# Optimization experiments

Measured on AMD Instinct MI355X. Metric: run time of the kernel, lower is better.

## Reference

```python
import jax, jax.numpy as jnp
import numpy as np

B, N, D = 2, 2048, 1024
H = 16
HD = D // H  # 64
N_CTX = 256


def setup_inputs() -> dict:
    key = jax.random.key(0)
    ks = jax.random.split(key, 10)
    x = jax.random.normal(ks[0], (B, N, D), dtype=jnp.float32)
    ctx_ppr = jax.random.uniform(ks[1], (N_CTX,), dtype=jnp.float32, minval=1e-4, maxval=1.0)
    ctx_trust = jax.random.uniform(ks[2], (N_CTX,), dtype=jnp.float32)
    attn_mask = jax.random.randint(ks[3], (N, N), 0, 2).astype(jnp.bool_)
    # parameters (nn.Linear convention: y = x @ W.T + b)
    s_in = 1.0 / np.sqrt(D)
    W_in = jax.random.uniform(ks[4], (3 * D, D), dtype=jnp.float32, minval=-s_in, maxval=s_in)
    b_in = jax.random.uniform(ks[5], (3 * D,), dtype=jnp.float32, minval=-s_in, maxval=s_in)
    W_out = jax.random.uniform(ks[6], (D, D), dtype=jnp.float32, minval=-s_in, maxval=s_in)
    b_out = jax.random.uniform(ks[7], (D,), dtype=jnp.float32, minval=-s_in, maxval=s_in)
    log_ppr_alpha = jnp.ones((1,), jnp.float32) * 0.1
    trust_scale = jnp.ones((1,), jnp.float32) * 0.1
    return {"x": x, "ctx_ppr": ctx_ppr, "ctx_trust": ctx_trust, "n_ctx": N_CTX,
            "attn_mask": attn_mask, "W_in": W_in, "b_in": b_in,
            "W_out": W_out, "b_out": b_out,
            "log_ppr_alpha": log_ppr_alpha, "trust_scale": trust_scale}


def reference(x, ctx_ppr, ctx_trust, n_ctx, attn_mask, W_in, b_in, W_out, b_out,
              log_ppr_alpha, trust_scale):
    Bx, Nx, Dx = x.shape
    scale = HD ** -0.5
    qkv = x @ W_in.T + b_in  # [B,N,3D]
    q, k, v = jnp.split(qkv, 3, axis=-1)
    q = q.reshape(Bx, Nx, H, HD).transpose(0, 2, 1, 3)  # [B,H,N,d]
    k = k.reshape(Bx, Nx, H, HD).transpose(0, 2, 1, 3)
    v = v.reshape(Bx, Nx, H, HD).transpose(0, 2, 1, 3)
    if n_ctx > 0:
        gate = jax.nn.sigmoid(trust_scale[0] * ctx_trust)  # [n_ctx]
        gate_full = jnp.concatenate([gate, jnp.ones(Nx - n_ctx, x.dtype)])
        v = v * gate_full[None, None, :, None]
    logits = jnp.einsum('bhqd,bhkd->bhqk', q, k) * scale
    if n_ctx > 0:
        bias = log_ppr_alpha[0] * jnp.log(jnp.clip(ctx_ppr, 1e-8, None))
        col_bias = jnp.concatenate([bias, jnp.zeros(Nx - n_ctx, x.dtype)])
        logits = logits + col_bias[None, None, None, :]
    logits = jnp.where(attn_mask[None, None, :, :], -jnp.inf, logits)
    weights = jax.nn.softmax(logits, axis=-1)
    out = jnp.einsum('bhqk,bhkd->bhqd', weights, v)
    out = out.transpose(0, 2, 1, 3).reshape(Bx, Nx, Dx)
    return out @ W_out.T + b_out
```

## Files before the change

### kernel.cpp

```cpp
#include <hip/hip_runtime.h>
#include <hip/hip_bf16.h>
#include <math.h>

#define B_   2
#define N_   2048
#define D_   1024
#define H_   16
#define TD_  3072
#define LOG2E 1.44269504088896340736f
#define SCALE_Q (0.125f * LOG2E)

typedef short  bf16x8 __attribute__((ext_vector_type(8)));
typedef _Float16 f16x8 __attribute__((ext_vector_type(8)));
typedef float  f32x4  __attribute__((ext_vector_type(4)));
typedef float  f32x16 __attribute__((ext_vector_type(16)));

#define MFMA16(a, b, c)   __builtin_amdgcn_mfma_f32_16x16x32_bf16(a, b, c, 0, 0, 0)
#define MFMA32B(a, b, c)  __builtin_amdgcn_mfma_f32_32x32x16_bf16(a, b, c, 0, 0, 0)
#define MFMA32H(a, b, c)  __builtin_amdgcn_mfma_f32_32x32x16_f16(a, b, c, 0, 0, 0)

__device__ __forceinline__ ushort f2bf(float f) {
    union { float f; unsigned u; } v; v.f = f;
    unsigned r = (v.u + 0x7fffu + ((v.u >> 16) & 1u)) >> 16;
    return (ushort)r;
}
__device__ __forceinline__ unsigned pkrtz(float a, float b) {
    typedef __fp16 h2 __attribute__((ext_vector_type(2)));
    union { h2 h; unsigned u; } c;
    c.h = __builtin_amdgcn_cvt_pkrtz(a, b);
    return c.u;
}
__device__ __forceinline__ void async16(const void* g, void* l) {
    __builtin_amdgcn_global_load_lds(
        (const __attribute__((address_space(1))) unsigned*)g,
        (__attribute__((address_space(3))) unsigned*)l, 16, 0, 0);
}

__global__ __launch_bounds__(256) void preprocess(
    const float* __restrict__ x, const float* __restrict__ W_in,
    const float* __restrict__ W_out, const float* __restrict__ ctx_ppr,
    const float* __restrict__ log_alpha, const int* __restrict__ n_ctx_p,
    const int* __restrict__ mask,
    ushort* __restrict__ xb, ushort* __restrict__ wib, ushort* __restrict__ wob,
    float* __restrict__ biasrow, unsigned* __restrict__ maskbits)
{
    const int J0 = 1048576, J1 = 786432, J2 = 262144, JM = 131072, JB = 2048;
    int t = blockIdx.x * 256 + threadIdx.x;
    if (t < J0 + J1 + J2) {
        const float* src; ushort* dst; int i = t;
        if (i < J0)           { src = x;      dst = xb;  }
        else if (i < J0 + J1) { i -= J0;      src = W_in;  dst = wib; }
        else                  { i -= J0 + J1; src = W_out; dst = wob; }
        float4 v = ((const float4*)src)[i];
        ushort4 o;
        o.x = f2bf(v.x); o.y = f2bf(v.y); o.z = f2bf(v.z); o.w = f2bf(v.w);
        ((ushort4*)dst)[i] = o;
    } else if (t < J0 + J1 + J2 + JM) {
        int i = t - (J0 + J1 + J2);
        const int4* m = (const int4*)(mask + (size_t)i * 32);
        unsigned bits = 0u;
        #pragma unroll
        for (int j = 0; j < 8; ++j) {
            int4 w = m[j];
            bits |= (w.x != 0 ? 1u : 0u) << (j * 4 + 0);
            bits |= (w.y != 0 ? 1u : 0u) << (j * 4 + 1);
            bits |= (w.z != 0 ? 1u : 0u) << (j * 4 + 2);
            bits |= (w.w != 0 ? 1u : 0u) << (j * 4 + 3);
        }
        maskbits[i] = bits;
    } else if (t < J0 + J1 + J2 + JM + JB) {
        int k = t - (J0 + J1 + J2 + JM);
        int nc = n_ctx_p[0];
        float bv = 0.f;
        if (k < nc) bv = log_alpha[0] * __log2f(fmaxf(ctx_ppr[k], 1e-8f));
        biasrow[k] = bv;
    }
}

template<int BCOL, int MODE>
__global__ __launch_bounds__(256) void gemm_bt(
    const ushort* __restrict__ A, const ushort* __restrict__ Bw,
    const float* __restrict__ bias, float* __restrict__ Cout,
    ushort* __restrict__ qkout, _Float16* __restrict__ vTout,
    int Ncol, int K,
    const float* __restrict__ ctx_trust, const float* __restrict__ trust_scale,
    const int* __restrict__ n_ctx_p)
{
    constexpr int NT = BCOL / 32;
    __shared__ ushort tA[128 * 32];
    __shared__ ushort tB[BCOL * 32];
    const int tid = threadIdx.x;
    const int lane = tid & 63, wv = tid >> 6;
    const int ln = lane & 15, kg = lane >> 4;
    const int rh = wv >> 1, ch = wv & 1;
    const int row0 = blockIdx.y * 128, col0 = blockIdx.x * BCOL;

    int offA[4], offB[NT];
    #pragma unroll
    for (int i = 0; i < 4; ++i) {
        int ra = rh * 64 + i * 16 + ln;
        offA[i] = ra * 32 + ((kg ^ ((ra >> 1) & 3)) << 3);
    }
    #pragma unroll
    for (int i = 0; i < NT; ++i) {
        int rb = ch * (BCOL / 2) + i * 16 + ln;
        offB[i] = rb * 32 + ((kg ^ ((rb >> 1) & 3)) << 3);
    }
    f32x4 acc[4][NT];
    #pragma unroll
    for (int i = 0; i < 4; ++i)
        #pragma unroll
        for (int j = 0; j < NT; ++j) acc[i][j] = (f32x4){0.f, 0.f, 0.f, 0.f};

    for (int kt = 0; kt < K; kt += 32) {
        __syncthreads();
        #pragma unroll
        for (int r2 = 0; r2 < 2; ++r2) {
            int g = r2 * 256 + tid;
            int row = g >> 2;
            int srck = ((g & 3) ^ ((row >> 1) & 3)) << 3;
            async16(A + (size_t)(row0 + row) * K + kt + srck, &tA[g * 8]);
        }
        #pragma unroll
        for (int r2 = 0; r2 < BCOL / 64; ++r2) {
            int g = r2 * 256 + tid;
            int row = g >> 2;
            int srck = ((g & 3) ^ ((row >> 1) & 3)) << 3;
            async16(Bw + (size_t)(col0 + row) * K + kt + srck, &tB[g * 8]);
        }
        __syncthreads();
        bf16x8 af[4], bfr[NT];
        #pragma unroll
        for (int i = 0; i < 4; ++i)  af[i]  = *(const bf16x8*)&tA[offA[i]];
        #pragma unroll
        for (int i = 0; i < NT; ++i) bfr[i] = *(const bf16x8*)&tB[offB[i]];
        #pragma unroll
        for (int mt = 0; mt < 4; ++mt)
            #pragma unroll
            for (int nt = 0; nt < NT; ++nt)
                acc[mt][nt] = MFMA16(af[mt], bfr[nt], acc[mt][nt]);
    }

    const int nctx = n_ctx_p ? n_ctx_p[0] : 0;
    const float ts = trust_scale ? trust_scale[0] : 0.f;
    #pragma unroll
    for (int nt = 0; nt < NT; ++nt) {
        int col = col0 + ch * (BCOL / 2) + nt * 16 + ln;
        float bv = bias[col];
        #pragma unroll
        for (int mt = 0; mt < 4; ++mt) {
            int rbase = row0 + rh * 64 + mt * 16 + kg * 4;
            f32x4 a = acc[mt][nt];
            if (MODE == 0) {
                #pragma unroll
                for (int reg = 0; reg < 4; ++reg)
                    Cout[(size_t)(rbase + reg) * Ncol + col] = a[reg] + bv;
            } else {
                if (col < D_) {
                    #pragma unroll
                    for (int reg = 0; reg < 4; ++reg)
                        qkout[(size_t)(rbase + reg) * 2048 + col] =
                            f2bf((a[reg] + bv) * SCALE_Q);
                } else if (col < 2 * D_) {
                    #pragma unroll
                    for (int reg = 0; reg < 4; ++reg)
                        qkout[(size_t)(rbase + reg) * 2048 + col] = f2bf(a[reg] + bv);
                } else {
                    int vc = col - 2 * D_;
                    int hh = vc >> 6, dim = vc & 63;
                    int bb = rbase >> 11, nbase = rbase & (N_ - 1);
                    ushort4 o;
                    #pragma unroll
                    for (int reg = 0; reg < 4; ++reg) {
                        float v = a[reg] + bv;
                        int n = nbase + reg;
                        if (n < nctx) {
                            float g = 1.f / (1.f + __expf(-ts * ctx_trust[n]));
                            v *= g;
                        }
                        _Float16 hv = (_Float16)v;
                        ((ushort*)&o)[reg] = *(ushort*)&hv;
                    }
                    *(ushort4*)&vTout[((size_t)(bb * 16 + hh) * 64 + dim) * 2048 + nbase] = o;
                }
            }
        }
    }
}

__global__ __launch_bounds__(256) void attn(
    const ushort* __restrict__ qkb,
    const _Float16* __restrict__ vT,
    const unsigned* __restrict__ maskbits,
    const float* __restrict__ biasrow,
    const int* __restrict__ n_ctx_p,
    ushort* __restrict__ attb)
{
    __shared__ ushort   Kt[2][64 * 64];
    __shared__ _Float16 Vt[2][64 * 64];
    const int tid = threadIdx.x;
    const int lane = tid & 63, wv = tid >> 6;
    const int q31 = lane & 31, hi = lane >> 5;
    const int b = blockIdx.y >> 4, h = blockIdx.y & 15;
    const int q0w = blockIdx.x * 128 + wv * 32;
    const int nctx = n_ctx_p[0];

    bf16x8 qf[4];
    {
        const ushort* qrow = qkb + (size_t)(b * N_ + q0w + q31) * 2048 + h * 64;
        #pragma unroll
        for (int ks = 0; ks < 4; ++ks)
            qf[ks] = *(const bf16x8*)(qrow + ks * 16 + hi * 8);
    }
    const size_t kgbase = (size_t)(b * N_) * 2048 + 1024 + h * 64;
    const _Float16* vbase = vT + (size_t)((b * 16 + h) * 64) * 2048;

    f32x16 O[2];
    O[0] = (f32x16)(0.f); O[1] = (f32x16)(0.f);
    float lrun = 0.f;

    {
        #pragma unroll
        for (int r2 = 0; r2 < 2; ++r2) {
            int g = r2 * 256 + tid; int row = g >> 3; int sg = (g & 7) ^ (row & 7);
            async16(qkb + kgbase + (size_t)row * 2048 + sg * 8, &Kt[0][g * 8]);
        }
        #pragma unroll
        for (int r2 = 0; r2 < 2; ++r2) {
            int g = r2 * 256 + tid; int row = g >> 3; int sg = (g & 7) ^ (row & 7);
            async16(vbase + (size_t)row * 2048 + sg * 8, &Vt[0][g * 8]);
        }
    }

    const int swz = q31 & 7;
    for (int ci = 0; ci < 32; ++ci) {
        const int c0 = ci * 64;
        __syncthreads();
        if (ci < 31) {
            const int c1 = c0 + 64, nb = (ci + 1) & 1;
            #pragma unroll
            for (int r2 = 0; r2 < 2; ++r2) {
                int g = r2 * 256 + tid; int row = g >> 3; int sg = (g & 7) ^ (row & 7);
                async16(qkb + kgbase + (size_t)(c1 + row) * 2048 + sg * 8, &Kt[nb][g * 8]);
            }
            #pragma unroll
            for (int r2 = 0; r2 < 2; ++r2) {
                int g = r2 * 256 + tid; int row = g >> 3; int sg = (g & 7) ^ (row & 7);
                async16(vbase + (size_t)row * 2048 + c1 + sg * 8, &Vt[nb][g * 8]);
            }
        }
        const ushort*   KT = Kt[ci & 1];
        const _Float16* VT = Vt[ci & 1];

        f32x16 S[2];
        S[0] = (f32x16)(0.f); S[1] = (f32x16)(0.f);
        #pragma unroll
        for (int t = 0; t < 2; ++t) {
            const int rbase = (t * 32 + q31) * 64;
            #pragma unroll
            for (int ks = 0; ks < 4; ++ks) {
                bf16x8 kf = *(const bf16x8*)&KT[rbase + (((ks * 2 + hi) ^ swz) << 3)];
                S[t] = MFMA32B(kf, qf[ks], S[t]);
            }
        }

        uint2 mw = *(const uint2*)&maskbits[(size_t)(q0w + q31) * 64 + ci * 2];
        unsigned msh[2] = { mw.x >> (hi * 4), mw.y >> (hi * 4) };
        unsigned pk[2][8];
        float lsum = 0.f;
        const bool has_bias = (c0 < nctx);
        #pragma unroll
        for (int t = 0; t < 2; ++t) {
            float p[16];
            #pragma unroll
            for (int g = 0; g < 4; ++g) {
                f32x4 bb = (f32x4){0.f, 0.f, 0.f, 0.f};
                if (has_bias)
                    bb = *(const f32x4*)&biasrow[c0 + t * 32 + g * 8 + hi * 4];
                #pragma unroll
                for (int r = 0; r < 4; ++r) {
                    const int reg = g * 4 + r;
                    const int br = r + 8 * g;
                    float s = S[t][reg] + bb[r] - 4.f;
                    s = ((msh[t] >> br) & 1u) ? -1e30f : s;
                    p[reg] = __builtin_exp2f(s);
                }
            }
            float l0 = (p[0] + p[1]) + (p[2] + p[3]);
            float l1 = (p[4] + p[5]) + (p[6] + p[7]);
            float l2 = (p[8] + p[9]) + (p[10] + p[11]);
            float l3 = (p[12] + p[13]) + (p[14] + p[15]);
            lsum += (l0 + l1) + (l2 + l3);
            #pragma unroll
            for (int i = 0; i < 8; ++i)
                pk[t][i] = pkrtz(p[2 * i], p[2 * i + 1]);
        }
        lrun += lsum;

        #pragma unroll
        for (int ks = 0; ks < 4; ++ks) {
            const int t = ks >> 1, lo4 = (ks & 1) * 4;
            unsigned u0 = pk[t][lo4 + 0], u1 = pk[t][lo4 + 1];
            unsigned u2 = pk[t][lo4 + 2], u3 = pk[t][lo4 + 3];
            unsigned own0 = hi ? u2 : u0, own1 = hi ? u3 : u1;
            unsigned snd0 = hi ? u0 : u2, snd1 = hi ? u1 : u3;
            unsigned rv0 = (unsigned)__shfl_xor((int)snd0, 32);
            unsigned rv1 = (unsigned)__shfl_xor((int)snd1, 32);
            union { f16x8 v; unsigned u[4]; } frag;
            frag.u[0] = hi ? rv0 : own0;
            frag.u[1] = hi ? rv1 : own1;
            frag.u[2] = hi ? own0 : rv0;
            frag.u[3] = hi ? own1 : rv1;
            #pragma unroll
            for (int t2 = 0; t2 < 2; ++t2) {
                const int vb = (t2 * 32 + q31) * 64;
                union { f16x8 v; int4 i; } vf;
                vf.i = *(const int4*)&VT[vb + (((ks * 2 + hi) ^ swz) << 3)];
                O[t2] = MFMA32H(vf.v, frag.v, O[t2]);
            }
        }
    }

    float l = lrun + __shfl_xor(lrun, 32);
    float inv = 1.f / l;
    ushort* orow = attb + (size_t)(b * N_ + q0w + q31) * 1024 + h * 64;
    #pragma unroll
    for (int t = 0; t < 2; ++t)
        #pragma unroll
        for (int g = 0; g < 4; ++g) {
            ushort4 o;
            #pragma unroll
            for (int r = 0; r < 4; ++r)
                ((ushort*)&o)[r] = f2bf(O[t][g * 4 + r] * inv);
            *(ushort4*)&orow[t * 32 + g * 8 + hi * 4] = o;
        }
}

extern "C" void kernel_launch(void* const* d_in, const int* in_sizes, int n_in,
                              void* d_out, int out_size, void* d_ws, size_t ws_size,
                              hipStream_t stream)
{
    const float* x         = (const float*)d_in[0];
    const float* ctx_ppr   = (const float*)d_in[1];
    const float* ctx_trust = (const float*)d_in[2];
    const int*   n_ctx_p   = (const int*)d_in[3];
    const int*   attn_mask = (const int*)d_in[4];
    const float* W_in      = (const float*)d_in[5];
    const float* b_in      = (const float*)d_in[6];
    const float* W_out     = (const float*)d_in[7];
    const float* b_out     = (const float*)d_in[8];
    const float* log_alpha = (const float*)d_in[9];
    const float* trust_sc  = (const float*)d_in[10];
    float* out = (float*)d_out;

    char* ws = (char*)d_ws;
    ushort*    xb       = (ushort*)ws;    ws += (size_t)4096 * 1024 * 2;
    ushort*    wib      = (ushort*)ws;    ws += (size_t)3072 * 1024 * 2;
    ushort*    wob      = (ushort*)ws;    ws += (size_t)1024 * 1024 * 2;
    ushort*    qkb      = (ushort*)ws;    ws += (size_t)4096 * 2048 * 2;
    _Float16*  vT       = (_Float16*)ws;  ws += (size_t)2048 * 2048 * 2;
    ushort*    attbuf   = (ushort*)ws;    ws += (size_t)4096 * 1024 * 2;
    float*     biasrow  = (float*)ws;     ws += 2048 * 4;
    unsigned*  maskbits = (unsigned*)ws;  ws += (size_t)2048 * 64 * 4;

    hipLaunchKernelGGL(preprocess, dim3(8712), dim3(256), 0, stream,
                       x, W_in, W_out, ctx_ppr, log_alpha, n_ctx_p, attn_mask,
                       xb, wib, wob, biasrow, maskbits);

    hipLaunchKernelGGL((gemm_bt<128, 1>), dim3(24, 32), dim3(256), 0, stream,
                       xb, wib, b_in, (float*)nullptr, qkb, vT, TD_, 1024,
                       ctx_trust, trust_sc, n_ctx_p);

    hipLaunchKernelGGL(attn, dim3(16, 32), dim3(256), 0, stream,
                       qkb, vT, maskbits, biasrow, n_ctx_p, attbuf);

    hipLaunchKernelGGL((gemm_bt<64, 0>), dim3(16, 32), dim3(256), 0, stream,
                       attbuf, wob, b_out, out, (ushort*)nullptr, (_Float16*)nullptr,
                       1024, 1024, ctx_trust, trust_sc, n_ctx_p);
}
```

Measured before the change: 268.7 us.

## Split attention over two key halves and merge partials in a combine kernel

```diff
diff --git a/kernel.cpp b/kernel.cpp
--- a/kernel.cpp
+++ b/kernel.cpp
@@ -12,6 +12,7 @@
 
 typedef short  bf16x8 __attribute__((ext_vector_type(8)));
 typedef _Float16 f16x8 __attribute__((ext_vector_type(8)));
+typedef _Float16 f16x4 __attribute__((ext_vector_type(4)));
 typedef float  f32x4  __attribute__((ext_vector_type(4)));
 typedef float  f32x16 __attribute__((ext_vector_type(16)));
 
@@ -34,6 +35,10 @@
     __builtin_amdgcn_global_load_lds(
         (const __attribute__((address_space(1))) unsigned*)g,
         (__attribute__((address_space(3))) unsigned*)l, 16, 0, 0);
+}
+__device__ __forceinline__ void plswap(unsigned &a, unsigned &b) {
+    auto r = __builtin_amdgcn_permlane32_swap((int)a, (int)b, false, false);
+    a = (unsigned)r[0]; b = (unsigned)r[1];
 }
 
 __global__ __launch_bounds__(256) void preprocess(
@@ -194,7 +199,9 @@
     const unsigned* __restrict__ maskbits,
     const float* __restrict__ biasrow,
     const int* __restrict__ n_ctx_p,
-    ushort* __restrict__ attb)
+    _Float16* __restrict__ op0,
+    _Float16* __restrict__ op1,
+    float* __restrict__ lpart)
 {
     __shared__ ushort   Kt[2][64 * 64];
     __shared__ _Float16 Vt[2][64 * 64];
@@ -203,6 +210,8 @@
     const int q31 = lane & 31, hi = lane >> 5;
     const int b = blockIdx.y >> 4, h = blockIdx.y & 15;
     const int q0w = blockIdx.x * 128 + wv * 32;
+    const int kh = blockIdx.z;
+    const int kbase = kh << 10;
     const int nctx = n_ctx_p[0];
 
     bf16x8 qf[4];
@@ -212,8 +221,8 @@
         for (int ks = 0; ks < 4; ++ks)
             qf[ks] = *(const bf16x8*)(qrow + ks * 16 + hi * 8);
     }
-    const size_t kgbase = (size_t)(b * N_) * 2048 + 1024 + h * 64;
-    const _Float16* vbase = vT + (size_t)((b * 16 + h) * 64) * 2048;
+    const size_t kgbase = (size_t)(b * N_ + kbase) * 2048 + 1024 + h * 64;
+    const _Float16* vbase = vT + (size_t)((b * 16 + h) * 64) * 2048 + kbase;
 
     f32x16 O[2];
     O[0] = (f32x16)(0.f); O[1] = (f32x16)(0.f);
@@ -233,10 +242,10 @@
     }
 
     const int swz = q31 & 7;
-    for (int ci = 0; ci < 32; ++ci) {
+    for (int ci = 0; ci < 16; ++ci) {
         const int c0 = ci * 64;
         __syncthreads();
-        if (ci < 31) {
+        if (ci < 15) {
             const int c1 = c0 + 64, nb = (ci + 1) & 1;
             #pragma unroll
             for (int r2 = 0; r2 < 2; ++r2) {
@@ -264,11 +273,12 @@
             }
         }
 
-        uint2 mw = *(const uint2*)&maskbits[(size_t)(q0w + q31) * 64 + ci * 2];
+        uint2 mw = *(const uint2*)&maskbits[(size_t)(q0w + q31) * 64 + (kbase >> 5) + ci * 2];
         unsigned msh[2] = { mw.x >> (hi * 4), mw.y >> (hi * 4) };
         unsigned pk[2][8];
         float lsum = 0.f;
-        const bool has_bias = (c0 < nctx);
+        const int c0g = kbase + c0;
+        const bool has_bias = (c0g < nctx);
         #pragma unroll
         for (int t = 0; t < 2; ++t) {
             float p[16];
@@ -276,7 +286,7 @@
             for (int g = 0; g < 4; ++g) {
                 f32x4 bb = (f32x4){0.f, 0.f, 0.f, 0.f};
                 if (has_bias)
-                    bb = *(const f32x4*)&biasrow[c0 + t * 32 + g * 8 + hi * 4];
+                    bb = *(const f32x4*)&biasrow[c0g + t * 32 + g * 8 + hi * 4];
                 #pragma unroll
                 for (int r = 0; r < 4; ++r) {
                     const int reg = g * 4 + r;
@@ -300,17 +310,13 @@
         #pragma unroll
         for (int ks = 0; ks < 4; ++ks) {
             const int t = ks >> 1, lo4 = (ks & 1) * 4;
-            unsigned u0 = pk[t][lo4 + 0], u1 = pk[t][lo4 + 1];
-            unsigned u2 = pk[t][lo4 + 2], u3 = pk[t][lo4 + 3];
-            unsigned own0 = hi ? u2 : u0, own1 = hi ? u3 : u1;
-            unsigned snd0 = hi ? u0 : u2, snd1 = hi ? u1 : u3;
-            unsigned rv0 = (unsigned)__shfl_xor((int)snd0, 32);
-            unsigned rv1 = (unsigned)__shfl_xor((int)snd1, 32);
+            unsigned w0 = pk[t][lo4 + 0], w1 = pk[t][lo4 + 1];
+            unsigned w2 = pk[t][lo4 + 2], w3 = pk[t][lo4 + 3];
+            plswap(w0, w2);
+            plswap(w1, w3);
             union { f16x8 v; unsigned u[4]; } frag;
-            frag.u[0] = hi ? rv0 : own0;
-            frag.u[1] = hi ? rv1 : own1;
-            frag.u[2] = hi ? own0 : rv0;
-            frag.u[3] = hi ? own1 : rv1;
+            frag.u[0] = w0; frag.u[1] = w1;
+            frag.u[2] = w2; frag.u[3] = w3;
             #pragma unroll
             for (int t2 = 0; t2 < 2; ++t2) {
                 const int vb = (t2 * 32 + q31) * 64;
@@ -323,17 +329,45 @@
 
     float l = lrun + __shfl_xor(lrun, 32);
     float inv = 1.f / l;
-    ushort* orow = attb + (size_t)(b * N_ + q0w + q31) * 1024 + h * 64;
+    _Float16* orow = (kh ? op1 : op0)
+                   + (size_t)(b * N_ + q0w + q31) * 1024 + h * 64;
     #pragma unroll
     for (int t = 0; t < 2; ++t)
         #pragma unroll
         for (int g = 0; g < 4; ++g) {
             ushort4 o;
             #pragma unroll
-            for (int r = 0; r < 4; ++r)
-                ((ushort*)&o)[r] = f2bf(O[t][g * 4 + r] * inv);
+            for (int r = 0; r < 4; ++r) {
+                _Float16 hv = (_Float16)(O[t][g * 4 + r] * inv);
+                ((ushort*)&o)[r] = *(ushort*)&hv;
+            }
             *(ushort4*)&orow[t * 32 + g * 8 + hi * 4] = o;
         }
+    if (hi == 0)
+        lpart[(kh << 16) + (b * 16 + h) * 2048 + q0w + q31] = l;
+}
+
+__global__ __launch_bounds__(256) void combine(
+    const _Float16* __restrict__ op0, const _Float16* __restrict__ op1,
+    const float* __restrict__ lpart, ushort* __restrict__ attb)
+{
+    int t = blockIdx.x * 256 + threadIdx.x;
+    size_t idx = (size_t)t * 4;
+    int col = (int)(idx & 1023);
+    int row = (int)(idx >> 10);
+    int h = col >> 6;
+    int b = row >> 11, q = row & 2047;
+    int lidx = (b * 16 + h) * 2048 + q;
+    float l0 = lpart[lidx], l1 = lpart[65536 + lidx];
+    float inv = 1.f / (l0 + l1);
+    float w0 = l0 * inv, w1 = l1 * inv;
+    f16x4 a0 = *(const f16x4*)(op0 + idx);
+    f16x4 a1 = *(const f16x4*)(op1 + idx);
+    ushort4 o;
+    #pragma unroll
+    for (int r = 0; r < 4; ++r)
+        ((ushort*)&o)[r] = f2bf((float)a0[r] * w0 + (float)a1[r] * w1);
+    *(ushort4*)(attb + idx) = o;
 }
 
 extern "C" void kernel_launch(void* const* d_in, const int* in_sizes, int n_in,
@@ -363,6 +397,10 @@
     float*     biasrow  = (float*)ws;     ws += 2048 * 4;
     unsigned*  maskbits = (unsigned*)ws;  ws += (size_t)2048 * 64 * 4;
 
+    _Float16* op0   = (_Float16*)xb;
+    _Float16* op1   = (_Float16*)attbuf;
+    float*    lpart = (float*)wib;
+
     hipLaunchKernelGGL(preprocess, dim3(8712), dim3(256), 0, stream,
                        x, W_in, W_out, ctx_ppr, log_alpha, n_ctx_p, attn_mask,
                        xb, wib, wob, biasrow, maskbits);
@@ -371,8 +409,11 @@
                        xb, wib, b_in, (float*)nullptr, qkb, vT, TD_, 1024,
                        ctx_trust, trust_sc, n_ctx_p);
 
-    hipLaunchKernelGGL(attn, dim3(16, 32), dim3(256), 0, stream,
-                       qkb, vT, maskbits, biasrow, n_ctx_p, attbuf);
+    hipLaunchKernelGGL(attn, dim3(16, 32, 2), dim3(256), 0, stream,
+                       qkb, vT, maskbits, biasrow, n_ctx_p, op0, op1, lpart);
+
+    hipLaunchKernelGGL(combine, dim3(4096), dim3(256), 0, stream,
+                       op0, op1, lpart, attbuf);
 
     hipLaunchKernelGGL((gemm_bt<64, 0>), dim3(16, 32), dim3(256), 0, stream,
                        attbuf, wob, b_out, out, (ushort*)nullptr, (_Float16*)nullptr,
```

After: 269.8 us. No clear change (+0.4%).
